# Performance work log

Hardware: AMD Instinct MI355X
Metric: run time of the kernel (lower is better)

## Reference

```python
import jax, jax.numpy as jnp
import numpy as np

B, S, HID = 1, 2048, 4096
H, HKV, D = 32, 8, 128
ROT = 64  # partial_rotary_factor = 0.5
EPS = 1e-6
SCALE = D ** -0.5


def setup_inputs() -> dict:
    key = jax.random.key(0)
    ks = jax.random.split(key, 8)
    return {
        "hidden_states": jax.random.normal(ks[0], (B, S, HID), jnp.float32),
        "cos": jax.random.uniform(ks[1], (B, S, ROT), jnp.float32),
        "sin": jax.random.uniform(ks[2], (B, S, ROT), jnp.float32),
        "Wq": jax.random.normal(ks[3], (H * D, HID), jnp.float32) * 0.02,
        "Wk": jax.random.normal(ks[4], (HKV * D, HID), jnp.float32) * 0.02,
        "Wv": jax.random.normal(ks[5], (HKV * D, HID), jnp.float32) * 0.02,
        "Wo": jax.random.normal(ks[6], (H * D, HID), jnp.float32).T * 0.02,  # [HID, H*D]
        "q_norm_w": jnp.ones((D,), jnp.float32),
        "k_norm_w": jnp.ones((D,), jnp.float32),
    }


def _rmsnorm(x, w):
    var = jnp.mean(jnp.square(x), axis=-1, keepdims=True)
    return x * jax.lax.rsqrt(var + EPS) * w


def _rotate_half(x):
    x1, x2 = jnp.split(x, 2, axis=-1)
    return jnp.concatenate([-x2, x1], axis=-1)


def reference(hidden_states, cos, sin, Wq, Wk, Wv, Wo, q_norm_w, k_norm_w):
    b, s, _ = hidden_states.shape
    q = (hidden_states @ Wq.T).reshape(b, s, H, D)
    k = (hidden_states @ Wk.T).reshape(b, s, HKV, D)
    v = (hidden_states @ Wv.T).reshape(b, s, HKV, D)
    # per-head QK RMSNorm
    q = _rmsnorm(q, q_norm_w)
    k = _rmsnorm(k, k_norm_w)
    # partial RoPE on first ROT dims; cos/sin broadcast over head dim (unsqueeze_dim=2)
    cs = cos[:, :, None, :]  # [B,S,1,ROT]
    sn = sin[:, :, None, :]
    q_rot, q_pass = q[..., :ROT], q[..., ROT:]
    k_rot, k_pass = k[..., :ROT], k[..., ROT:]
    q_rot = q_rot * cs + _rotate_half(q_rot) * sn
    k_rot = k_rot * cs + _rotate_half(k_rot) * sn
    q = jnp.concatenate([q_rot, q_pass], axis=-1)
    k = jnp.concatenate([k_rot, k_pass], axis=-1)
    # GQA: expand kv heads to query heads
    rep = H // HKV
    k = jnp.repeat(k, rep, axis=2)  # [B,S,H,D]
    v = jnp.repeat(v, rep, axis=2)
    # causal SDPA, bsnd layout
    scores = jnp.einsum("bqhd,bkhd->bhqk", q, k) * SCALE
    causal = jnp.tril(jnp.ones((s, s), bool))
    scores = jnp.where(causal, scores, jnp.finfo(scores.dtype).min)
    attn = jax.nn.softmax(scores, axis=-1)
    out = jnp.einsum("bhqk,bkhd->bqhd", attn, v).reshape(b, s, H * D)
    return out @ Wo.T
```

## Files before the change

### kernel.cpp

```cpp
#include <hip/hip_runtime.h>
#include <hip/hip_bf16.h>

typedef __attribute__((ext_vector_type(8))) short bf16x8;
typedef __attribute__((ext_vector_type(4))) float f32x4;
typedef __hip_bfloat16 bf16;

#define S_LEN 2048
#define HIDDEN 4096
#define NH 32
#define NKV 8
#define DH 128
#define ROTD 64
#define QKVW 6144
#define KOFF 4096
#define VOFF 5120
#define ATT_SCALE 0.08838834764831845f
#define RMS_EPS 1e-6f
#define KPITCH 136
#define VPITCH 72

#define BAR() __builtin_amdgcn_s_barrier()
#define VMCNT(n) asm volatile("s_waitcnt vmcnt(" #n ")" ::: "memory")
#define LGKM(n)  asm volatile("s_waitcnt lgkmcnt(" #n ")" ::: "memory")

static __device__ __forceinline__ unsigned short f2bu(float f) {
    bf16 h = __float2bfloat16(f);
    return __builtin_bit_cast(unsigned short, h);
}

static __device__ __forceinline__ void load_lds_16(const bf16* g, bf16* l) {
    __builtin_amdgcn_global_load_lds((const __attribute__((address_space(1))) void*)g,
                                     (__attribute__((address_space(3))) void*)l, 16, 0, 0);
}

__global__ __launch_bounds__(256) void cast_f32_bf16(const float* __restrict__ src,
                                                     unsigned short* __restrict__ dst, int n4) {
    int i = blockIdx.x * 256 + threadIdx.x;
    if (i >= n4) return;
    float4 v = reinterpret_cast<const float4*>(src)[i];
    ushort4 o;
    o.x = f2bu(v.x); o.y = f2bu(v.y); o.z = f2bu(v.z); o.w = f2bu(v.w);
    reinterpret_cast<ushort4*>(dst)[i] = o;
}

#define LDA_SUB(bufi, half) do {                                                        \
    const bf16* _ab = &As[bufi][half][0];                                               \
    _Pragma("unroll") for (int mf = 0; mf < 4; ++mf) {                                  \
        const int _r = arow + mf * 16;                                                  \
        _Pragma("unroll") for (int kk = 0; kk < 2; ++kk)                                \
            av[mf][kk] = *reinterpret_cast<const bf16x8*>(                              \
                _ab + (((_r << 6) + kk * 32 + quad * 8) ^ xorv));                       \
    } } while (0)

#define LDB_SUB(bufi, half, set) do {                                                   \
    const bf16* _bb = &Bs[bufi][half][0];                                               \
    _Pragma("unroll") for (int nf = 0; nf < 2; ++nf) {                                  \
        const int _r = brow + nf * 16;                                                  \
        _Pragma("unroll") for (int kk = 0; kk < 2; ++kk)                                \
            bv[set][nf][kk] = *reinterpret_cast<const bf16x8*>(                         \
                _bb + (((_r << 6) + kk * 32 + quad * 8) ^ xorv));                       \
    } } while (0)

#define MMQ(mh, nh, set) do {                                                           \
    _Pragma("unroll") for (int mf = 0; mf < 4; ++mf)                                    \
    _Pragma("unroll") for (int nf = 0; nf < 2; ++nf)                                    \
    _Pragma("unroll") for (int kk = 0; kk < 2; ++kk)                                    \
        acc[mh][nh][mf][nf] = __builtin_amdgcn_mfma_f32_16x16x32_bf16(                  \
            av[mf][kk], bv[set][nf][kk], acc[mh][nh][mf][nf], 0, 0, 0);                 \
    } while (0)

#define STAGE_A(bufi, half, tau) do {                                                   \
    const bf16* _s = Abase + (size_t)(half) * 128 * K + (size_t)(tau) * 64;             \
    load_lds_16(_s + sro0, &As[bufi][half][e0]);                                        \
    load_lds_16(_s + sro1, &As[bufi][half][e1]); } while (0)

#define STAGE_B(bufi, half, tau) do {                                                   \
    const bf16* _s = Bbase + (size_t)(half) * 128 * K + (size_t)(tau) * 64;             \
    load_lds_16(_s + sro0, &Bs[bufi][half][e0]);                                        \
    load_lds_16(_s + sro1, &Bs[bufi][half][e1]); } while (0)

template <typename OutT>
__global__ __launch_bounds__(512, 2) void gemm256(const bf16* __restrict__ A,
                                                  const bf16* __restrict__ B,
                                                  OutT* __restrict__ C,
                                                  int M, int N, int K) {
    __shared__ bf16 As[2][2][128 * 64];
    __shared__ bf16 Bs[2][2][128 * 64];

    const int tid  = threadIdx.x;
    const int lane = tid & 63;
    const int lq   = lane & 15;
    const int quad = lane >> 4;
    const int wave = tid >> 6;
    const int wr   = wave >> 2;
    const int wc   = wave & 3;

    const int nwg = gridDim.x;
    const int cpx = nwg >> 3;
    const int wg  = (blockIdx.x & 7) * cpx + (blockIdx.x >> 3);
    const int ntn = N >> 8;
    const int m0  = (wg / ntn) << 8;
    const int n0  = (wg % ntn) << 8;

    const int NT = K >> 6;

    const int d0 = tid * 16;
    const int d1 = 8192 + tid * 16;
    const int o0 = d0 ^ (((d0 >> 7) & 7) << 4);
    const int o1 = d1 ^ (((d1 >> 7) & 7) << 4);
    const int e0 = d0 >> 1;
    const int e1 = d1 >> 1;
    const size_t sro0 = (size_t)((o0 >> 1) >> 6) * K + ((o0 >> 1) & 63);
    const size_t sro1 = (size_t)((o1 >> 1) >> 6) * K + ((o1 >> 1) & 63);
    const bf16* Abase = A + (size_t)m0 * K;
    const bf16* Bbase = B + (size_t)n0 * K;

    const int arow = wr * 64 + lq;
    const int brow = wc * 32 + lq;
    const int xorv = (lq & 7) << 3;

    f32x4  acc[2][2][4][2] = {};
    bf16x8 av[4][2];
    bf16x8 bv[2][2][2];

    STAGE_B(0, 0, 0); STAGE_A(0, 0, 0); STAGE_B(0, 1, 0); STAGE_A(0, 1, 0);
    STAGE_B(1, 0, 1); STAGE_A(1, 0, 1); STAGE_B(1, 1, 1);
    VMCNT(6);
    BAR();

    for (int t = 0; t < NT; ++t) {
        const int buf = t & 1;

        LDA_SUB(buf, 0);
        LDB_SUB(buf, 0, 0);
        if (t + 1 < NT) STAGE_A(buf ^ 1, 1, t + 1);
        LGKM(8);
        BAR();
        LGKM(0);
        __builtin_amdgcn_s_setprio(1);
        MMQ(0, 0, 0);
        __builtin_amdgcn_s_setprio(0);
        BAR();

        LDB_SUB(buf, 1, 1);
        if (t + 2 < NT) STAGE_B(buf, 0, t + 2);
        BAR();
        LGKM(0);
        __builtin_amdgcn_s_setprio(1);
        MMQ(0, 1, 1);
        __builtin_amdgcn_s_setprio(0);
        BAR();

        LDA_SUB(buf, 1);
        if (t + 2 < NT) STAGE_A(buf, 0, t + 2);
        BAR();
        LGKM(0);
        __builtin_amdgcn_s_setprio(1);
        MMQ(1, 1, 1);
        __builtin_amdgcn_s_setprio(0);
        BAR();

        if (t + 2 < NT) STAGE_B(buf, 1, t + 2);
        BAR();
        __builtin_amdgcn_s_setprio(1);
        MMQ(1, 0, 0);
        __builtin_amdgcn_s_setprio(0);
        if (t < NT - 2) { VMCNT(6); } else { VMCNT(0); }
        BAR();
    }

#pragma unroll
    for (int mh = 0; mh < 2; ++mh)
#pragma unroll
        for (int nh = 0; nh < 2; ++nh)
#pragma unroll
            for (int mf = 0; mf < 4; ++mf)
#pragma unroll
                for (int nf = 0; nf < 2; ++nf)
#pragma unroll
                    for (int r = 0; r < 4; ++r) {
                        const int row = m0 + mh * 128 + wr * 64 + mf * 16 + quad * 4 + r;
                        const int col = n0 + nh * 128 + wc * 32 + nf * 16 + lq;
                        const float v = acc[mh][nh][mf][nf][r];
                        const size_t idx = (size_t)row * N + col;
                        if constexpr (sizeof(OutT) == 2) C[idx] = __float2bfloat16(v);
                        else                             C[idx] = v;
                    }
}

__global__ __launch_bounds__(256) void norm_rope(bf16* __restrict__ buf,
                                                 const float* __restrict__ w,
                                                 const float* __restrict__ cosp,
                                                 const float* __restrict__ sinp,
                                                 int log2nh, int stride, int coloff) {
    const int lane = threadIdx.x & 63;
    const int wave = threadIdx.x >> 6;
    const int row  = blockIdx.x * 4 + wave;
    const int s    = row >> log2nh;
    const int hh   = row & ((1 << log2nh) - 1);
    bf16* p = buf + (size_t)s * stride + coloff + hh * DH;

    float x1 = __bfloat162float(p[lane]);
    float x2 = __bfloat162float(p[64 + lane]);

    float ss = x1 * x1 + x2 * x2;
#pragma unroll
    for (int off = 1; off < 64; off <<= 1) ss += __shfl_xor(ss, off);
    float rs = rsqrtf(ss * (1.0f / 128.0f) + RMS_EPS);

    float y1 = x1 * rs * w[lane];
    float y2 = x2 * rs * w[64 + lane];

    float partner = __shfl_xor(y1, 32);
    float c  = cosp[(size_t)s * ROTD + lane];
    float sn = sinp[(size_t)s * ROTD + lane];
    float rot = (lane < 32) ? (y1 * c - partner * sn) : (y1 * c + partner * sn);

    p[lane]      = __float2bfloat16(rot);
    p[64 + lane] = __float2bfloat16(y2);
}

__global__ __launch_bounds__(256) void transpose_v(const bf16* __restrict__ v,
                                                   bf16* __restrict__ vt,
                                                   int stride, int colofs) {
    __shared__ bf16 t[32][65];
    const int c0 = blockIdx.x * 32;
    const int s0 = blockIdx.y * 64;
    {
        const int j  = threadIdx.x & 31;
        const int i0 = threadIdx.x >> 5;
#pragma unroll
        for (int p = 0; p < 8; ++p) {
            int si = p * 8 + i0;
            t[j][si] = v[(size_t)(s0 + si) * stride + colofs + c0 + j];
        }
    }
    __syncthreads();
    {
        const int ii = threadIdx.x & 63;
        const int j0 = threadIdx.x >> 6;
#pragma unroll
        for (int p = 0; p < 8; ++p) {
            int c = p * 4 + j0;
            vt[(size_t)(c0 + c) * S_LEN + s0 + ii] = t[c][ii];
        }
    }
}

struct FlashSmem {
    bf16 Ks[64][KPITCH];
    bf16 Vs[128][VPITCH];
    bf16 Ps[4][16][VPITCH];
};

static __device__ __forceinline__ void attn_qblock(int q0, int n_iter, int h, int kvh,
                                                   const bf16* __restrict__ QKV,
                                                   const bf16* __restrict__ VT,
                                                   bf16* __restrict__ O,
                                                   FlashSmem* sm) {
    const int tid  = threadIdx.x;
    const int lane = tid & 63;
    const int wave = tid >> 6;
    const int lq   = lane & 15;
    const int quad = lane >> 4;
    const int qr0  = q0 + wave * 16;

    bf16x8 qf[4];
    const bf16* qrow = QKV + (size_t)(qr0 + lq) * QKVW + h * DH + quad * 8;
#pragma unroll
    for (int i = 0; i < 4; ++i) {
        bf16x8 qv = *reinterpret_cast<const bf16x8*>(qrow + 32 * i);
#pragma unroll
        for (int j = 0; j < 8; ++j) {
            bf16 b = __builtin_bit_cast(bf16, (unsigned short)qv[j]);
            qv[j] = (short)__builtin_bit_cast(unsigned short,
                        __float2bfloat16(__bfloat162float(b) * ATT_SCALE));
        }
        qf[i] = qv;
    }

    f32x4 o[8];
#pragma unroll
    for (int t2 = 0; t2 < 8; ++t2) o[t2] = (f32x4){0.f, 0.f, 0.f, 0.f};
    float m_i[4], l_i[4];
#pragma unroll
    for (int r = 0; r < 4; ++r) { m_i[r] = -1e30f; l_i[r] = 0.f; }

    const bf16* kg = QKV + (size_t)(tid >> 2) * QKVW + KOFF + kvh * DH + (tid & 3) * 32;
    const bf16* vg = VT + (size_t)(kvh * DH + (tid >> 1)) * S_LEN + (tid & 1) * 32;
    bf16* ksl = &sm->Ks[tid >> 2][(tid & 3) * 32];
    bf16* vsl = &sm->Vs[tid >> 1][(tid & 1) * 32];
    bf16* pb  = &sm->Ps[wave][0][0];

    bf16x8 kreg[4], vreg[4];
#pragma unroll
    for (int c = 0; c < 4; ++c) {
        kreg[c] = *reinterpret_cast<const bf16x8*>(kg + 8 * c);
        vreg[c] = *reinterpret_cast<const bf16x8*>(vg + 8 * c);
    }

    for (int kt = 0; kt < n_iter; ++kt) {
        const int k0 = kt * 64;
#pragma unroll
        for (int c = 0; c < 4; ++c) {
            *reinterpret_cast<bf16x8*>(ksl + 8 * c) = kreg[c];
            *reinterpret_cast<bf16x8*>(vsl + 8 * c) = vreg[c];
        }
        __syncthreads();
        if (kt + 1 < n_iter) {
            const size_t kadv = (size_t)(kt + 1) * 64;
#pragma unroll
            for (int c = 0; c < 4; ++c) {
                kreg[c] = *reinterpret_cast<const bf16x8*>(kg + kadv * QKVW + 8 * c);
                vreg[c] = *reinterpret_cast<const bf16x8*>(vg + kadv + 8 * c);
            }
        }

        float p[4][4];
#pragma unroll
        for (int t = 0; t < 4; ++t) {
            f32x4 sacc = (f32x4){0.f, 0.f, 0.f, 0.f};
#pragma unroll
            for (int i = 0; i < 4; ++i) {
                bf16x8 kf = *reinterpret_cast<const bf16x8*>(&sm->Ks[t * 16 + lq][quad * 8 + 32 * i]);
                sacc = __builtin_amdgcn_mfma_f32_16x16x32_bf16(qf[i], kf, sacc, 0, 0, 0);
            }
#pragma unroll
            for (int r = 0; r < 4; ++r) {
                int qi = qr0 + quad * 4 + r;
                int ki = k0 + t * 16 + lq;
                p[t][r] = (ki > qi) ? -1e30f : sacc[r];
            }
        }

        float rowmax[4];
#pragma unroll
        for (int r = 0; r < 4; ++r)
            rowmax[r] = fmaxf(fmaxf(p[0][r], p[1][r]), fmaxf(p[2][r], p[3][r]));
#pragma unroll
        for (int off = 1; off < 16; off <<= 1)
#pragma unroll
            for (int r = 0; r < 4; ++r) rowmax[r] = fmaxf(rowmax[r], __shfl_xor(rowmax[r], off));

        float alpha[4];
#pragma unroll
        for (int r = 0; r < 4; ++r) {
            float mn = fmaxf(m_i[r], rowmax[r]);
            alpha[r] = __expf(m_i[r] - mn);
            m_i[r] = mn;
        }
#pragma unroll
        for (int t = 0; t < 4; ++t)
#pragma unroll
            for (int r = 0; r < 4; ++r) p[t][r] = __expf(p[t][r] - m_i[r]);

        float rsum[4];
#pragma unroll
        for (int r = 0; r < 4; ++r) rsum[r] = (p[0][r] + p[1][r]) + (p[2][r] + p[3][r]);
#pragma unroll
        for (int off = 1; off < 16; off <<= 1)
#pragma unroll
            for (int r = 0; r < 4; ++r) rsum[r] += __shfl_xor(rsum[r], off);
#pragma unroll
        for (int r = 0; r < 4; ++r) l_i[r] = l_i[r] * alpha[r] + rsum[r];

#pragma unroll
        for (int t = 0; t < 4; ++t)
#pragma unroll
            for (int r = 0; r < 4; ++r)
                pb[(quad * 4 + r) * VPITCH + t * 16 + lq] = __float2bfloat16(p[t][r]);
        __threadfence_block();

#pragma unroll
        for (int t2 = 0; t2 < 8; ++t2)
#pragma unroll
            for (int r = 0; r < 4; ++r) o[t2][r] *= alpha[r];

#pragma unroll
        for (int hh = 0; hh < 2; ++hh) {
            bf16x8 pa = *reinterpret_cast<const bf16x8*>(pb + lq * VPITCH + hh * 32 + quad * 8);
#pragma unroll
            for (int t2 = 0; t2 < 8; ++t2) {
                bf16x8 vf = *reinterpret_cast<const bf16x8*>(&sm->Vs[t2 * 16 + lq][hh * 32 + quad * 8]);
                o[t2] = __builtin_amdgcn_mfma_f32_16x16x32_bf16(pa, vf, o[t2], 0, 0, 0);
            }
        }
        __syncthreads();
    }

#pragma unroll
    for (int r = 0; r < 4; ++r) l_i[r] = 1.0f / l_i[r];
#pragma unroll
    for (int t2 = 0; t2 < 8; ++t2)
#pragma unroll
        for (int r = 0; r < 4; ++r)
            O[(size_t)(qr0 + quad * 4 + r) * (NH * DH) + h * DH + t2 * 16 + lq] =
                __float2bfloat16(o[t2][r] * l_i[r]);
}

__global__ __launch_bounds__(256) void flash_attn(const bf16* __restrict__ QKV,
                                                  const bf16* __restrict__ VT,
                                                  bf16* __restrict__ O) {
    __shared__ FlashSmem sm;
    const int b  = blockIdx.x;
    const int h  = b & 31;
    const int pr = b >> 5;
    const int kvh = h >> 2;
    attn_qblock((31 - pr) * 64, 32 - pr, h, kvh, QKV, VT, O, &sm);
    __syncthreads();
    attn_qblock(pr * 64,        pr + 1,  h, kvh, QKV, VT, O, &sm);
}

extern "C" void kernel_launch(void* const* d_in, const int* in_sizes, int n_in,
                              void* d_out, int out_size, void* d_ws, size_t ws_size,
                              hipStream_t stream) {
    const float* hs   = (const float*)d_in[0];
    const float* cosp = (const float*)d_in[1];
    const float* sinp = (const float*)d_in[2];
    const float* Wq   = (const float*)d_in[3];
    const float* Wk   = (const float*)d_in[4];
    const float* Wv   = (const float*)d_in[5];
    const float* Wo   = (const float*)d_in[6];
    const float* qw   = (const float*)d_in[7];
    const float* kw   = (const float*)d_in[8];
    float* out = (float*)d_out;

    char* ws = (char*)d_ws;
    size_t off = 0;
    auto carve = [&](size_t bytes) { char* p = ws + off; off += (bytes + 255) & ~(size_t)255; return p; };

    bf16* hsb  = (bf16*)carve((size_t)S_LEN * HIDDEN * 2);
    bf16* wqkv = (bf16*)carve((size_t)QKVW * HIDDEN * 2);
    bf16* wob  = (bf16*)carve((size_t)HIDDEN * NH * DH * 2);
    bf16* qkv  = (bf16*)carve((size_t)S_LEN * QKVW * 2);
    bf16* vtb  = (bf16*)carve((size_t)NKV * DH * S_LEN * 2);

    cast_f32_bf16<<<(S_LEN * HIDDEN / 4 + 255) / 256, 256, 0, stream>>>(hs, (unsigned short*)hsb, S_LEN * HIDDEN / 4);
    cast_f32_bf16<<<(NH * DH * HIDDEN / 4 + 255) / 256, 256, 0, stream>>>(Wq, (unsigned short*)wqkv, NH * DH * HIDDEN / 4);
    cast_f32_bf16<<<(NKV * DH * HIDDEN / 4 + 255) / 256, 256, 0, stream>>>(Wk, (unsigned short*)(wqkv + (size_t)KOFF * HIDDEN), NKV * DH * HIDDEN / 4);
    cast_f32_bf16<<<(NKV * DH * HIDDEN / 4 + 255) / 256, 256, 0, stream>>>(Wv, (unsigned short*)(wqkv + (size_t)VOFF * HIDDEN), NKV * DH * HIDDEN / 4);
    cast_f32_bf16<<<(HIDDEN * NH * DH / 4 + 255) / 256, 256, 0, stream>>>(Wo, (unsigned short*)wob, HIDDEN * NH * DH / 4);

    gemm256<bf16><<<dim3((S_LEN / 256) * (QKVW / 256)), 512, 0, stream>>>(hsb, wqkv, qkv, S_LEN, QKVW, HIDDEN);

    norm_rope<<<S_LEN * NH / 4, 256, 0, stream>>>(qkv, qw, cosp, sinp, 5, QKVW, 0);
    norm_rope<<<S_LEN * NKV / 4, 256, 0, stream>>>(qkv, kw, cosp, sinp, 3, QKVW, KOFF);

    transpose_v<<<dim3(NKV * DH / 32, S_LEN / 64), 256, 0, stream>>>(qkv, vtb, QKVW, VOFF);

    bf16* aob = hsb;
    flash_attn<<<512, 256, 0, stream>>>(qkv, vtb, aob);

    gemm256<float><<<dim3((S_LEN / 256) * (HIDDEN / 256)), 512, 0, stream>>>(aob, wob, out, S_LEN, HIDDEN, NH * DH);
}
```

Before: 563.0 us.

## Software-pipeline LDS fragment loads across GEMM tiles with double-buffered registers

Restructures the bf16 GEMM main loop so that LDS-to-register fragment loads for the next quarter or next k-tile are issued before the MFMA block of the current quarter, using separate register sets (a0/a0n/a1, b0/b0n/b1). The loop is unrolled by two to ping-pong register sets, and sched_barrier is used to stop the compiler from reordering. Explicit lgkmcnt waits are removed and the vmcnt thresholds are retuned. The aim is to hide LDS read latency behind matrix ops, at the cost of higher register pressure at 2 waves/SIMD. It also assumes NT is even, and correctness depends on the vmcnt/barrier accounting being right.

```diff
diff --git a/kernel.cpp b/kernel.cpp
--- a/kernel.cpp
+++ b/kernel.cpp
@@ -20,8 +20,8 @@
 #define VPITCH 72
 
 #define BAR() __builtin_amdgcn_s_barrier()
+#define SB0() __builtin_amdgcn_sched_barrier(0)
 #define VMCNT(n) asm volatile("s_waitcnt vmcnt(" #n ")" ::: "memory")
-#define LGKM(n)  asm volatile("s_waitcnt lgkmcnt(" #n ")" ::: "memory")
 
 static __device__ __forceinline__ unsigned short f2bu(float f) {
     bf16 h = __float2bfloat16(f);
@@ -43,30 +43,30 @@
     reinterpret_cast<ushort4*>(dst)[i] = o;
 }
 
-#define LDA_SUB(bufi, half) do {                                                        \
+#define LDAH(bufi, half, dst) do {                                                      \
     const bf16* _ab = &As[bufi][half][0];                                               \
     _Pragma("unroll") for (int mf = 0; mf < 4; ++mf) {                                  \
         const int _r = arow + mf * 16;                                                  \
         _Pragma("unroll") for (int kk = 0; kk < 2; ++kk)                                \
-            av[mf][kk] = *reinterpret_cast<const bf16x8*>(                              \
+            dst[mf][kk] = *reinterpret_cast<const bf16x8*>(                             \
                 _ab + (((_r << 6) + kk * 32 + quad * 8) ^ xorv));                       \
     } } while (0)
 
-#define LDB_SUB(bufi, half, set) do {                                                   \
+#define LDBH(bufi, half, dst) do {                                                      \
     const bf16* _bb = &Bs[bufi][half][0];                                               \
     _Pragma("unroll") for (int nf = 0; nf < 2; ++nf) {                                  \
         const int _r = brow + nf * 16;                                                  \
         _Pragma("unroll") for (int kk = 0; kk < 2; ++kk)                                \
-            bv[set][nf][kk] = *reinterpret_cast<const bf16x8*>(                         \
+            dst[nf][kk] = *reinterpret_cast<const bf16x8*>(                             \
                 _bb + (((_r << 6) + kk * 32 + quad * 8) ^ xorv));                       \
     } } while (0)
 
-#define MMQ(mh, nh, set) do {                                                           \
+#define MMQ(mh, nh, A_, B_) do {                                                        \
     _Pragma("unroll") for (int mf = 0; mf < 4; ++mf)                                    \
     _Pragma("unroll") for (int nf = 0; nf < 2; ++nf)                                    \
     _Pragma("unroll") for (int kk = 0; kk < 2; ++kk)                                    \
         acc[mh][nh][mf][nf] = __builtin_amdgcn_mfma_f32_16x16x32_bf16(                  \
-            av[mf][kk], bv[set][nf][kk], acc[mh][nh][mf][nf], 0, 0, 0);                 \
+            A_[mf][kk], B_[nf][kk], acc[mh][nh][mf][nf], 0, 0, 0);                      \
     } while (0)
 
 #define STAGE_A(bufi, half, tau) do {                                                   \
@@ -78,6 +78,43 @@
     const bf16* _s = Bbase + (size_t)(half) * 128 * K + (size_t)(tau) * 64;             \
     load_lds_16(_s + sro0, &Bs[bufi][half][e0]);                                        \
     load_lds_16(_s + sro1, &Bs[bufi][half][e1]); } while (0)
+
+#define TILE(tconst, bufc, AC, BC, AN, BN_) do {                                        \
+    const int _t = (tconst);                                                            \
+    const bool _tail = (_t >= NT - 3);                                                  \
+              \
+    if (_tail) { VMCNT(0); } else { VMCNT(8); }                                         \
+    if (_t + 1 < NT) STAGE_A((bufc) ^ 1, 1, _t + 1);                                    \
+    BAR(); SB0();                                                                       \
+    LDBH(bufc, 1, b1);                                                                  \
+    __builtin_amdgcn_s_setprio(1); MMQ(0, 0, AC, BC);                                   \
+    __builtin_amdgcn_s_setprio(0);                                                      \
+    BAR();                                                                              \
+                               \
+    if (_tail) { VMCNT(0); } else { VMCNT(8); }                                         \
+    if (_t + 2 < NT) STAGE_B(bufc, 0, _t + 2);                                          \
+    BAR(); SB0();                                                                       \
+    LDAH(bufc, 1, a1);                                                                  \
+    __builtin_amdgcn_s_setprio(1); MMQ(0, 1, AC, b1);                                   \
+    __builtin_amdgcn_s_setprio(0);                                                      \
+    BAR();                                                                              \
+                           \
+    if (_tail) { VMCNT(0); } else { VMCNT(6); }                                         \
+    if (_t + 2 < NT) STAGE_A(bufc, 0, _t + 2);                                          \
+    BAR(); SB0();                                                                       \
+    if (_t + 1 < NT) LDAH((bufc) ^ 1, 0, AN);                                           \
+    __builtin_amdgcn_s_setprio(1); MMQ(1, 1, a1, b1);                                   \
+    __builtin_amdgcn_s_setprio(0);                                                      \
+    BAR();                                                                              \
+                           \
+    if (_tail) { VMCNT(0); } else { VMCNT(10); }                                        \
+    if (_t + 2 < NT) STAGE_B(bufc, 1, _t + 2);                                          \
+    BAR(); SB0();                                                                       \
+    if (_t + 1 < NT) LDBH((bufc) ^ 1, 0, BN_);                                          \
+    __builtin_amdgcn_s_setprio(1); MMQ(1, 0, a1, BC);                                   \
+    __builtin_amdgcn_s_setprio(0);                                                      \
+    BAR();                                                                              \
+} while (0)
 
 template <typename OutT>
 __global__ __launch_bounds__(512, 2) void gemm256(const bf16* __restrict__ A,
@@ -120,53 +157,19 @@
     const int xorv = (lq & 7) << 3;
 
     f32x4  acc[2][2][4][2] = {};
-    bf16x8 av[4][2];
-    bf16x8 bv[2][2][2];
+    bf16x8 a0[4][2], a0n[4][2], a1[4][2];
+    bf16x8 b0[2][2], b0n[2][2], b1[2][2];
 
     STAGE_B(0, 0, 0); STAGE_A(0, 0, 0); STAGE_B(0, 1, 0); STAGE_A(0, 1, 0);
     STAGE_B(1, 0, 1); STAGE_A(1, 0, 1); STAGE_B(1, 1, 1);
-    VMCNT(6);
-    BAR();
-
-    for (int t = 0; t < NT; ++t) {
-        const int buf = t & 1;
-
-        LDA_SUB(buf, 0);
-        LDB_SUB(buf, 0, 0);
-        if (t + 1 < NT) STAGE_A(buf ^ 1, 1, t + 1);
-        LGKM(8);
-        BAR();
-        LGKM(0);
-        __builtin_amdgcn_s_setprio(1);
-        MMQ(0, 0, 0);
-        __builtin_amdgcn_s_setprio(0);
-        BAR();
-
-        LDB_SUB(buf, 1, 1);
-        if (t + 2 < NT) STAGE_B(buf, 0, t + 2);
-        BAR();
-        LGKM(0);
-        __builtin_amdgcn_s_setprio(1);
-        MMQ(0, 1, 1);
-        __builtin_amdgcn_s_setprio(0);
-        BAR();
-
-        LDA_SUB(buf, 1);
-        if (t + 2 < NT) STAGE_A(buf, 0, t + 2);
-        BAR();
-        LGKM(0);
-        __builtin_amdgcn_s_setprio(1);
-        MMQ(1, 1, 1);
-        __builtin_amdgcn_s_setprio(0);
-        BAR();
-
-        if (t + 2 < NT) STAGE_B(buf, 1, t + 2);
-        BAR();
-        __builtin_amdgcn_s_setprio(1);
-        MMQ(1, 0, 0);
-        __builtin_amdgcn_s_setprio(0);
-        if (t < NT - 2) { VMCNT(6); } else { VMCNT(0); }
-        BAR();
+    VMCNT(10);
+    BAR(); SB0();
+    LDAH(0, 0, a0);
+    LDBH(0, 0, b0);
+
+    for (int tt = 0; tt < NT; tt += 2) {
+        TILE(tt,     0, a0,  b0,  a0n, b0n);
+        TILE(tt + 1, 1, a0n, b0n, a0,  b0);
     }
 
 #pragma unroll
```

Measured after the change: 1.703 ms. +202.5%, slower.
